# Kernel tuning notes

Hardware: AMD Instinct MI355X
Metric: run time of the kernel (lower is better)

Reference implementation:

```python
import jax, jax.numpy as jnp
import numpy as np

N = 100000      # nodes
E = 1600000     # edges (avg degree 16)
F_IN = 128
H = 64
OUT = 1
NEG_SLOPE = 0.2  # PyG GATConv default negative_slope


def setup_inputs() -> dict:
    key = jax.random.key(0)
    ks = jax.random.split(key, 20)
    inp = {
        "x": jax.random.normal(ks[0], (N, F_IN), dtype=jnp.float32),
        "edge_index": jax.random.randint(ks[1], (2, E), 0, N, dtype=jnp.int64),
        "edge_weight": jax.random.uniform(ks[2], (E,), dtype=jnp.float32),
    }
    # GATConv params: W [in,out], att_src [out], att_dst [out], bias [out]
    dims = [(F_IN, H), (H, H), (H, H), (H, OUT)]
    names = ["0", "1", "2", "l"]
    ki = 3
    for nm, (fi, fo) in zip(names, dims):
        s = 1.0 / np.sqrt(fi)
        inp["W" + nm] = jax.random.normal(ks[ki], (fi, fo), dtype=jnp.float32) * s; ki += 1
        inp["as" + nm] = jax.random.normal(ks[ki], (fo,), dtype=jnp.float32) * 0.1; ki += 1
        inp["ad" + nm] = jax.random.normal(ks[ki], (fo,), dtype=jnp.float32) * 0.1; ki += 1
        inp["b" + nm] = jnp.zeros((fo,), dtype=jnp.float32)
    return inp


def gat_conv(x, src, dst, W, a_s, a_d, b, n):
    # h = W x  (single head)
    h = x @ W                                   # [N, F_out]
    e_src = h @ a_s                             # [N] per-node src attention term
    e_dst = h @ a_d                             # [N] per-node dst attention term
    e = jax.nn.leaky_relu(e_src[src] + e_dst[dst], NEG_SLOPE)   # [E+N]
    # segment softmax over incoming edges of each dst node (self-loops ensure non-empty)
    m = jax.ops.segment_max(e, dst, num_segments=n)
    ex = jnp.exp(e - m[dst])
    denom = jax.ops.segment_sum(ex, dst, num_segments=n)
    alpha = ex / (denom[dst] + 1e-16)
    # scatter-add aggregation of alpha-weighted source features
    out = jax.ops.segment_sum(h[src] * alpha[:, None], dst, num_segments=n)
    return out + b


def reference(x, edge_index, edge_weight,
              W0, as0, ad0, b0,
              W1, as1, ad1, b1,
              W2, as2, ad2, b2,
              Wl, asl, adl, bl):
    # eval mode: F.dropout(training=False) is identity; edge_weight unused by GATConv
    n = x.shape[0]
    loop = jnp.arange(n, dtype=edge_index.dtype)
    src = jnp.concatenate([edge_index[0], loop])   # add_self_loops=True
    dst = jnp.concatenate([edge_index[1], loop])
    for (W, a_s, a_d, b) in [(W0, as0, ad0, b0), (W1, as1, ad1, b1), (W2, as2, ad2, b2)]:
        x = jax.nn.relu(gat_conv(x, src, dst, W, a_s, a_d, b, n))
    return gat_conv(x, src, dst, Wl, asl, adl, bl, n)
```

## Files before the change

kernel.cpp:

```cpp
#include <hip/hip_runtime.h>
#include <hip/hip_bf16.h>
#include <math.h>

#define CAP 64

typedef __attribute__((ext_vector_type(8))) short bf16x8;
typedef __attribute__((ext_vector_type(4))) float f32x4;

__device__ __forceinline__ short f2b(float f) {
    unsigned u = __float_as_uint(f);
    unsigned r = (u + 0x7FFFu + ((u >> 16) & 1u)) >> 16;
    return (short)r;
}
__device__ __forceinline__ float b2f(short b) {
    return __uint_as_float(((unsigned)(unsigned short)b) << 16);
}


__global__ __launch_bounds__(256) void fill_part_kernel(
        const int* __restrict__ ei, int* __restrict__ deg,
        int* __restrict__ col, int E, float pscale) {
    int part = blockIdx.x & 7;
    int chunk = blockIdx.x >> 3;
    int nchunk = gridDim.x >> 3;
    int per = (E + nchunk - 1) / nchunk;
    int lo = chunk * per;
    int hi = lo + per; if (hi > E) hi = E;
    for (int idx = lo + threadIdx.x; idx < hi; idx += 256) {
        int d = ei[E + idx];
        int pd = (int)((float)d * pscale); if (pd > 7) pd = 7;
        if (pd == part) {
            int s = ei[idx];
            int pos = atomicAdd(&deg[d], 1);
            if (pos < CAP - 1) col[(size_t)d * CAP + pos] = s;
        }
    }
}


template<int K>
__global__ __launch_bounds__(256) void gemm_mfma_kernel(
        const float* __restrict__ x, const float* __restrict__ W,
        const float* __restrict__ a_s, const float* __restrict__ a_d,
        float* __restrict__ h, float* __restrict__ es, float* __restrict__ ed, int n) {
    constexpr int NK = K / 32;
    __shared__ short bfrag[2 * 4 * NK * 64 * 8];
    constexpr int HALF = 4 * NK * 64 * 8;

    int tid = threadIdx.x;
    int lane = tid & 63;
    int l15 = lane & 15;
    int lg = lane >> 4;

    if (tid < 64) {
        for (int nf = 0; nf < 4; ++nf) {
            for (int ks = 0; ks < NK; ++ks) {
                int base = ((nf * NK + ks) * 64 + lane) * 8;
                #pragma unroll
                for (int j = 0; j < 8; ++j) {
                    float wv = W[(ks * 32 + lg * 8 + j) * 64 + nf * 16 + l15];
                    short hb = f2b(wv);
                    bfrag[base + j] = hb;
                    bfrag[HALF + base + j] = f2b(wv - b2f(hb));
                }
            }
        }
    }
    __syncthreads();

    float asv[4], adv[4];
    #pragma unroll
    for (int nf = 0; nf < 4; ++nf) {
        asv[nf] = a_s[nf * 16 + l15];
        adv[nf] = a_d[nf * 16 + l15];
    }

    int wid = (blockIdx.x * 256 + tid) >> 6;
    int nw = (gridDim.x * 256) >> 6;
    int ntiles = (n + 15) / 16;

    for (int t = wid; t < ntiles; t += nw) {
        int row0 = t * 16;
        int row = row0 + l15; if (row >= n) row = n - 1;
        const float* xr = x + (size_t)row * K + lg * 8;

        bf16x8 ahi[NK], alo[NK];
        #pragma unroll
        for (int ks = 0; ks < NK; ++ks) {
            float4 v0 = *(const float4*)(xr + ks * 32);
            float4 v1 = *(const float4*)(xr + ks * 32 + 4);
            float xv[8] = {v0.x, v0.y, v0.z, v0.w, v1.x, v1.y, v1.z, v1.w};
            #pragma unroll
            for (int j = 0; j < 8; ++j) {
                short hb = f2b(xv[j]);
                ahi[ks][j] = hb;
                alo[ks][j] = f2b(xv[j] - b2f(hb));
            }
        }

        f32x4 accs[4];
        #pragma unroll
        for (int nf = 0; nf < 4; ++nf) {
            f32x4 acc = {0.f, 0.f, 0.f, 0.f};
            #pragma unroll
            for (int ks = 0; ks < NK; ++ks) {
                bf16x8 bh = *(bf16x8*)&bfrag[((nf * NK + ks) * 64 + lane) * 8];
                bf16x8 bl = *(bf16x8*)&bfrag[HALF + ((nf * NK + ks) * 64 + lane) * 8];
                acc = __builtin_amdgcn_mfma_f32_16x16x32_bf16(ahi[ks], bh, acc, 0, 0, 0);
                acc = __builtin_amdgcn_mfma_f32_16x16x32_bf16(ahi[ks], bl, acc, 0, 0, 0);
                acc = __builtin_amdgcn_mfma_f32_16x16x32_bf16(alo[ks], bh, acc, 0, 0, 0);
            }
            accs[nf] = acc;
        }

        #pragma unroll
        for (int r = 0; r < 4; ++r) {
            int orow = row0 + lg * 4 + r;
            float ps = 0.f, pd = 0.f;
            if (orow < n) {
                #pragma unroll
                for (int nf = 0; nf < 4; ++nf) {
                    float hv = accs[nf][r];
                    h[(size_t)orow * 64 + nf * 16 + l15] = hv;
                    ps = fmaf(hv, asv[nf], ps);
                    pd = fmaf(hv, adv[nf], pd);
                }
            }
            #pragma unroll
            for (int off = 8; off; off >>= 1) {
                ps += __shfl_xor(ps, off);
                pd += __shfl_xor(pd, off);
            }
            if (l15 == 0 && orow < n) { es[orow] = ps; ed[orow] = pd; }
        }
    }
}


template<bool PROJ>
__global__ __launch_bounds__(256) void aggregate64_kernel(
        const float* __restrict__ h, const float* __restrict__ es, const float* __restrict__ ed,
        const int* __restrict__ deg, const int* __restrict__ col,
        const float* __restrict__ bias, float* __restrict__ xout, int n, int do_relu,
        const float* __restrict__ Wl, float* __restrict__ hl) {
    int lane = threadIdx.x & 63;
    int node = (blockIdx.x * blockDim.x + threadIdx.x) >> 6;
    if (node >= n) return;
    int cr = deg[node]; if (cr > CAP - 1) cr = CAP - 1;
    int cnt = cr + 1;
    float edi = ed[node];

    int s = 0;
    float e = -INFINITY;
    if (lane < cr) {
        s = col[(size_t)node * CAP + lane];
        float t = es[s] + edi;
        e = (t >= 0.f) ? t : 0.2f * t;
    } else if (lane == cr) {
        s = node;
        float t = es[node] + edi;
        e = (t >= 0.f) ? t : 0.2f * t;
    }
    float m = e;
    #pragma unroll
    for (int off = 32; off; off >>= 1) m = fmaxf(m, __shfl_xor(m, off));
    float p = __expf(e - m);
    float denom = p;
    #pragma unroll
    for (int off = 32; off; off >>= 1) denom += __shfl_xor(denom, off);

    float a0 = 0.f, a1 = 0.f, a2 = 0.f, a3 = 0.f;
    float a4 = 0.f, a5 = 0.f, a6 = 0.f, a7 = 0.f;
    int iters = (cnt + 7) & ~7;
    for (int j = 0; j < iters; j += 8) {
        float p0 = __shfl(p, j + 0); int s0 = __shfl(s, j + 0);
        float p1 = __shfl(p, j + 1); int s1 = __shfl(s, j + 1);
        float p2 = __shfl(p, j + 2); int s2 = __shfl(s, j + 2);
        float p3 = __shfl(p, j + 3); int s3 = __shfl(s, j + 3);
        float p4 = __shfl(p, j + 4); int s4 = __shfl(s, j + 4);
        float p5 = __shfl(p, j + 5); int s5 = __shfl(s, j + 5);
        float p6 = __shfl(p, j + 6); int s6 = __shfl(s, j + 6);
        float p7 = __shfl(p, j + 7); int s7 = __shfl(s, j + 7);
        a0 = fmaf(p0, h[(s0 << 6) | lane], a0);
        a1 = fmaf(p1, h[(s1 << 6) | lane], a1);
        a2 = fmaf(p2, h[(s2 << 6) | lane], a2);
        a3 = fmaf(p3, h[(s3 << 6) | lane], a3);
        a4 = fmaf(p4, h[(s4 << 6) | lane], a4);
        a5 = fmaf(p5, h[(s5 << 6) | lane], a5);
        a6 = fmaf(p6, h[(s6 << 6) | lane], a6);
        a7 = fmaf(p7, h[(s7 << 6) | lane], a7);
    }
    float o = (((a0 + a1) + (a2 + a3)) + ((a4 + a5) + (a6 + a7))) / denom + bias[lane];
    if (do_relu) o = fmaxf(o, 0.f);
    if constexpr (PROJ) {
        float ph = o * Wl[lane];
        #pragma unroll
        for (int off = 32; off; off >>= 1) ph += __shfl_xor(ph, off);
        if (lane == 0) hl[node] = ph;
    } else {
        xout[(size_t)node * 64 + lane] = o;
    }
}


__global__ __launch_bounds__(256) void aggregate1_kernel(
        const float* __restrict__ hl, const float* __restrict__ asl,
        const float* __restrict__ adl, const float* __restrict__ bl,
        const int* __restrict__ deg, const int* __restrict__ col,
        float* __restrict__ out, int n) {
    int lane = threadIdx.x & 63;
    int node = (blockIdx.x * blockDim.x + threadIdx.x) >> 6;
    if (node >= n) return;
    float As = asl[0], Ad = adl[0], B = bl[0];
    int cr = deg[node]; if (cr > CAP - 1) cr = CAP - 1;
    float edi = hl[node] * Ad;

    float hs = 0.f;
    float e = -INFINITY;
    if (lane < cr) {
        int s = col[(size_t)node * CAP + lane];
        hs = hl[s];
        float t = fmaf(hs, As, edi);
        e = (t >= 0.f) ? t : 0.2f * t;
    } else if (lane == cr) {
        hs = hl[node];
        float t = fmaf(hs, As, edi);
        e = (t >= 0.f) ? t : 0.2f * t;
    }
    float m = e;
    #pragma unroll
    for (int off = 32; off; off >>= 1) m = fmaxf(m, __shfl_xor(m, off));
    float p = __expf(e - m);
    float d = p;
    float a = p * hs;
    #pragma unroll
    for (int off = 32; off; off >>= 1) {
        d += __shfl_xor(d, off);
        a += __shfl_xor(a, off);
    }
    if (lane == 0) out[node] = a / d + B;
}


extern "C" void kernel_launch(void* const* d_in, const int* in_sizes, int n_in,
                              void* d_out, int out_size, void* d_ws, size_t ws_size,
                              hipStream_t stream) {
    const float* x0  = (const float*)d_in[0];
    const int*   ei  = (const int*)d_in[1];
    const float* W0  = (const float*)d_in[3];
    const float* as0 = (const float*)d_in[4];
    const float* ad0 = (const float*)d_in[5];
    const float* b0  = (const float*)d_in[6];
    const float* W1  = (const float*)d_in[7];
    const float* as1 = (const float*)d_in[8];
    const float* ad1 = (const float*)d_in[9];
    const float* b1  = (const float*)d_in[10];
    const float* W2  = (const float*)d_in[11];
    const float* as2 = (const float*)d_in[12];
    const float* ad2 = (const float*)d_in[13];
    const float* b2  = (const float*)d_in[14];
    const float* Wl  = (const float*)d_in[15];
    const float* asl = (const float*)d_in[16];
    const float* adl = (const float*)d_in[17];
    const float* bl  = (const float*)d_in[18];

    int n = in_sizes[0] / 128;
    int E = in_sizes[1] / 2;

    char* p = (char*)d_ws;
    auto alloc = [&](size_t bytes) { char* r = p; p += (bytes + 255) & ~255ULL; return r; };
    float* h   = (float*)alloc((size_t)n * 64 * 4);
    float* xb  = (float*)alloc((size_t)n * 64 * 4);
    int*   col = (int*)alloc((size_t)n * CAP * 4);
    float* es  = (float*)alloc((size_t)n * 4);
    float* ed  = (float*)alloc((size_t)n * 4);
    float* hl  = (float*)alloc((size_t)n * 4);
    int*   deg = (int*)alloc((size_t)n * 4);
    (void)ws_size; (void)n_in; (void)out_size;

    int agg_blocks = (n + 3) / 4;
    int ntiles = (n + 15) / 16;
    int gemm_blocks = (ntiles + 3) / 4;

    hipMemsetAsync(deg, 0, (size_t)n * 4, stream);
    fill_part_kernel<<<8 * 512, 256, 0, stream>>>(ei, deg, col, E, 8.0f / (float)n);

    gemm_mfma_kernel<128><<<gemm_blocks, 256, 0, stream>>>(x0, W0, as0, ad0, h, es, ed, n);
    aggregate64_kernel<false><<<agg_blocks, 256, 0, stream>>>(h, es, ed, deg, col, b0,
                                                              xb, n, 1, nullptr, nullptr);
    gemm_mfma_kernel<64><<<gemm_blocks, 256, 0, stream>>>(xb, W1, as1, ad1, h, es, ed, n);
    aggregate64_kernel<false><<<agg_blocks, 256, 0, stream>>>(h, es, ed, deg, col, b1,
                                                              xb, n, 1, nullptr, nullptr);
    gemm_mfma_kernel<64><<<gemm_blocks, 256, 0, stream>>>(xb, W2, as2, ad2, h, es, ed, n);
    aggregate64_kernel<true><<<agg_blocks, 256, 0, stream>>>(h, es, ed, deg, col, b2,
                                                             nullptr, n, 1, Wl, hl);
    aggregate1_kernel<<<agg_blocks, 256, 0, stream>>>(hl, asl, adl, bl, deg, col,
                                                      (float*)d_out, n);
}
```

Measured before the change: 371.5 us.

## Fuse CSR fill and first-layer GEMM into one launch to overlap them

Merges the edge-bucketing fill kernel and the first-layer MFMA GEMM into a single kernel. The first FB blocks do the partitioned atomic fill and the remaining blocks run the GEMM, so the two independent stages can share the GPU at once instead of running back to back. It also switches the edge-index reads to nontemporal loads. The cost is that every block now reserves the GEMM's shared-memory footprint, including the fill blocks, which may reduce occupancy for the atomic-heavy fill phase.

```diff
diff --git a/kernel.cpp b/kernel.cpp
--- a/kernel.cpp
+++ b/kernel.cpp
@@ -17,22 +17,122 @@
 }
 
 
-__global__ __launch_bounds__(256) void fill_part_kernel(
-        const int* __restrict__ ei, int* __restrict__ deg,
-        int* __restrict__ col, int E, float pscale) {
-    int part = blockIdx.x & 7;
-    int chunk = blockIdx.x >> 3;
-    int nchunk = gridDim.x >> 3;
-    int per = (E + nchunk - 1) / nchunk;
-    int lo = chunk * per;
-    int hi = lo + per; if (hi > E) hi = E;
-    for (int idx = lo + threadIdx.x; idx < hi; idx += 256) {
-        int d = ei[E + idx];
-        int pd = (int)((float)d * pscale); if (pd > 7) pd = 7;
-        if (pd == part) {
-            int s = ei[idx];
-            int pos = atomicAdd(&deg[d], 1);
-            if (pos < CAP - 1) col[(size_t)d * CAP + pos] = s;
+template<int K>
+__global__ __launch_bounds__(256) void fill_gemm_kernel(
+        const int* __restrict__ ei, int* __restrict__ deg, int* __restrict__ col,
+        int E, float pscale, int FB,
+        const float* __restrict__ x, const float* __restrict__ W,
+        const float* __restrict__ a_s, const float* __restrict__ a_d,
+        float* __restrict__ h, float* __restrict__ es, float* __restrict__ ed, int n) {
+    constexpr int NK = K / 32;
+    __shared__ short bfrag[2 * 4 * NK * 64 * 8];
+    constexpr int HALF = 4 * NK * 64 * 8;
+
+    int tid = threadIdx.x;
+
+    if ((int)blockIdx.x < FB) {
+        int part = blockIdx.x & 7;
+        int chunk = blockIdx.x >> 3;
+        int nchunk = FB >> 3;
+        int per = (E + nchunk - 1) / nchunk;
+        int lo = chunk * per;
+        int hi = lo + per; if (hi > E) hi = E;
+        for (int idx = lo + tid; idx < hi; idx += 256) {
+            int d = __builtin_nontemporal_load(ei + E + idx);
+            int pd = (int)((float)d * pscale); if (pd > 7) pd = 7;
+            if (pd == part) {
+                int s = __builtin_nontemporal_load(ei + idx);
+                int pos = atomicAdd(&deg[d], 1);
+                if (pos < CAP - 1) col[(size_t)d * CAP + pos] = s;
+            }
+        }
+        return;
+    }
+
+    int lane = tid & 63;
+    int l15 = lane & 15;
+    int lg = lane >> 4;
+
+    if (tid < 64) {
+        for (int nf = 0; nf < 4; ++nf) {
+            for (int ks = 0; ks < NK; ++ks) {
+                int base = ((nf * NK + ks) * 64 + lane) * 8;
+                #pragma unroll
+                for (int j = 0; j < 8; ++j) {
+                    float wv = W[(ks * 32 + lg * 8 + j) * 64 + nf * 16 + l15];
+                    short hb = f2b(wv);
+                    bfrag[base + j] = hb;
+                    bfrag[HALF + base + j] = f2b(wv - b2f(hb));
+                }
+            }
+        }
+    }
+    __syncthreads();
+
+    float asv[4], adv[4];
+    #pragma unroll
+    for (int nf = 0; nf < 4; ++nf) {
+        asv[nf] = a_s[nf * 16 + l15];
+        adv[nf] = a_d[nf * 16 + l15];
+    }
+
+    int wid = (((int)blockIdx.x - FB) * 256 + tid) >> 6;
+    int nw = ((gridDim.x - FB) * 256) >> 6;
+    int ntiles = (n + 15) / 16;
+
+    for (int t = wid; t < ntiles; t += nw) {
+        int row0 = t * 16;
+        int row = row0 + l15; if (row >= n) row = n - 1;
+        const float* xr = x + (size_t)row * K + lg * 8;
+
+        bf16x8 ahi[NK], alo[NK];
+        #pragma unroll
+        for (int ks = 0; ks < NK; ++ks) {
+            float4 v0 = *(const float4*)(xr + ks * 32);
+            float4 v1 = *(const float4*)(xr + ks * 32 + 4);
+            float xv[8] = {v0.x, v0.y, v0.z, v0.w, v1.x, v1.y, v1.z, v1.w};
+            #pragma unroll
+            for (int j = 0; j < 8; ++j) {
+                short hb = f2b(xv[j]);
+                ahi[ks][j] = hb;
+                alo[ks][j] = f2b(xv[j] - b2f(hb));
+            }
+        }
+
+        f32x4 accs[4];
+        #pragma unroll
+        for (int nf = 0; nf < 4; ++nf) {
+            f32x4 acc = {0.f, 0.f, 0.f, 0.f};
+            #pragma unroll
+            for (int ks = 0; ks < NK; ++ks) {
+                bf16x8 bh = *(bf16x8*)&bfrag[((nf * NK + ks) * 64 + lane) * 8];
+                bf16x8 bl = *(bf16x8*)&bfrag[HALF + ((nf * NK + ks) * 64 + lane) * 8];
+                acc = __builtin_amdgcn_mfma_f32_16x16x32_bf16(ahi[ks], bh, acc, 0, 0, 0);
+                acc = __builtin_amdgcn_mfma_f32_16x16x32_bf16(ahi[ks], bl, acc, 0, 0, 0);
+                acc = __builtin_amdgcn_mfma_f32_16x16x32_bf16(alo[ks], bh, acc, 0, 0, 0);
+            }
+            accs[nf] = acc;
+        }
+
+        #pragma unroll
+        for (int r = 0; r < 4; ++r) {
+            int orow = row0 + lg * 4 + r;
+            float ps = 0.f, pd = 0.f;
+            if (orow < n) {
+                #pragma unroll
+                for (int nf = 0; nf < 4; ++nf) {
+                    float hv = accs[nf][r];
+                    h[(size_t)orow * 64 + nf * 16 + l15] = hv;
+                    ps = fmaf(hv, asv[nf], ps);
+                    pd = fmaf(hv, adv[nf], pd);
+                }
+            }
+            #pragma unroll
+            for (int off = 8; off; off >>= 1) {
+                ps += __shfl_xor(ps, off);
+                pd += __shfl_xor(pd, off);
+            }
+            if (l15 == 0 && orow < n) { es[orow] = ps; ed[orow] = pd; }
         }
     }
 }
@@ -281,11 +381,13 @@
     int agg_blocks = (n + 3) / 4;
     int ntiles = (n + 15) / 16;
     int gemm_blocks = (ntiles + 3) / 4;
+    int FB = 8 * 512;
 
     hipMemsetAsync(deg, 0, (size_t)n * 4, stream);
-    fill_part_kernel<<<8 * 512, 256, 0, stream>>>(ei, deg, col, E, 8.0f / (float)n);
-
-    gemm_mfma_kernel<128><<<gemm_blocks, 256, 0, stream>>>(x0, W0, as0, ad0, h, es, ed, n);
+
+    fill_gemm_kernel<128><<<FB + gemm_blocks, 256, 0, stream>>>(
+        ei, deg, col, E, 8.0f / (float)n, FB,
+        x0, W0, as0, ad0, h, es, ed, n);
     aggregate64_kernel<false><<<agg_blocks, 256, 0, stream>>>(h, es, ed, deg, col, b0,
                                                               xb, n, 1, nullptr, nullptr);
     gemm_mfma_kernel<64><<<gemm_blocks, 256, 0, stream>>>(xb, W1, as1, ad1, h, es, ed, n);
```

Measured after the change: 457.8 us. +23.2%, slower.
